# Optimization experiments

Measured on AMD Instinct MI355X. Metric: run time of the kernel, lower is better.

The kernel has to match this reference:

```python
import jax, jax.numpy as jnp
import numpy as np

N = 50000   # total nodes (50 graphs x 1000 nodes)
E = 500000  # total edges (avg degree 10)
G = 50      # number of graphs in the batch
IN = 128    # in_dim
H = 4       # attn_head
HID = [64, 128]  # graph_hiddens
SLOPE = 0.2      # negative_slope


def setup_inputs() -> dict:
    key = jax.random.key(0)
    ks = jax.random.split(key, 12)
    nodes_per_g = N // G
    edges_per_g = E // G
    # edges stay inside their own graph block (batched-graph structure)
    off = (jnp.arange(E) // edges_per_g) * nodes_per_g
    edge_src = (jax.random.randint(ks[0], (E,), 0, nodes_per_g) + off).astype(jnp.int32)
    edge_dst = (jax.random.randint(ks[1], (E,), 0, nodes_per_g) + off).astype(jnp.int32)
    node_graph = (jnp.arange(N) // nodes_per_g).astype(jnp.int32)

    def lin(k, i, o):
        return (jax.random.normal(k, (i, o), jnp.float32) / np.sqrt(i)).astype(jnp.float32)

    return dict(
        x=jax.random.normal(ks[2], (N, IN), jnp.float32),
        edge_src=edge_src, edge_dst=edge_dst, node_graph=node_graph,
        Wl1=lin(ks[3], IN, H * HID[0]), bl1=jnp.zeros((H * HID[0],), jnp.float32),
        Wr1=lin(ks[4], IN, H * HID[0]), br1=jnp.zeros((H * HID[0],), jnp.float32),
        attn1=jax.random.normal(ks[5], (H, HID[0]), jnp.float32) * 0.1,
        Wl2=lin(ks[6], HID[0], H * HID[1]), bl2=jnp.zeros((H * HID[1],), jnp.float32),
        Wr2=lin(ks[7], HID[0], H * HID[1]), br2=jnp.zeros((H * HID[1],), jnp.float32),
        attn2=jax.random.normal(ks[8], (H, HID[1]), jnp.float32) * 0.1,
        gate_w=lin(ks[9], HID[1], 1), gate_b=jnp.zeros((1,), jnp.float32),
    )


def _gat_layer(x, src, dst, Wl, bl, Wr, br, attn, n_heads, d_out):
    """DGL GATv2Conv (share_weights=False, no dropout) + maxpool over heads."""
    n = x.shape[0]
    fs = (x @ Wl + bl).reshape(n, n_heads, d_out)  # fc_src -> [N,H,D]
    fd = (x @ Wr + br).reshape(n, n_heads, d_out)  # fc_dst -> [N,H,D]
    # per-edge GATv2 logits: attn . leaky_relu(fs_u + fd_v)
    e = jax.nn.leaky_relu(fs[src] + fd[dst], SLOPE)      # [E,H,D]
    logits = jnp.einsum('ehd,hd->eh', e, attn)           # [E,H]
    # edge softmax over incoming edges of each destination node
    m = jax.ops.segment_max(logits, dst, num_segments=n)  # [N,H]
    a = jnp.exp(logits - m[dst])
    s = jax.ops.segment_sum(a, dst, num_segments=n)
    alpha = a / s[dst]                                   # [E,H]
    out = jax.ops.segment_sum(alpha[:, :, None] * fs[src], dst, num_segments=n)  # [N,H,D]
    # MaxPool1d(attn_head) over the head dimension -> [N,D]
    return out.max(axis=1)


def reference(x, edge_src, edge_dst, node_graph,
              Wl1, bl1, Wr1, br1, attn1,
              Wl2, bl2, Wr2, br2, attn2,
              gate_w, gate_b):
    h = _gat_layer(x, edge_src, edge_dst, Wl1, bl1, Wr1, br1, attn1, H, HID[0])
    h = _gat_layer(h, edge_src, edge_dst, Wl2, bl2, Wr2, br2, attn2, H, HID[1])
    # GlobalAttentionPooling: softmax(gate_nn(h)) per graph, weighted sum
    gate = (h @ gate_w + gate_b)[:, 0]                      # [N]
    gm = jax.ops.segment_max(gate, node_graph, num_segments=G)
    ga = jnp.exp(gate - gm[node_graph])
    gs = jax.ops.segment_sum(ga, node_graph, num_segments=G)
    alpha = (ga / gs[node_graph])[:, None]                  # [N,1]
    return jax.ops.segment_sum(alpha * h, node_graph, num_segments=G)  # [G, HID[1]]
```

## Files before the change

### kernel.cpp

```cpp
#include <hip/hip_runtime.h>
#include <hip/hip_bf16.h>


#define NN 50000
#define EE 500000
#define GG 50
#define NPG 1000
#define HH 4
#define NB_E ((EE + 255) / 256)
#define NB_W 512

typedef unsigned short ushort_t;
typedef unsigned int uint_t;
typedef __attribute__((ext_vector_type(8))) short bf16x8;
typedef __attribute__((ext_vector_type(4))) float f32x4;
typedef __attribute__((ext_vector_type(2))) float f32x2;

__device__ __forceinline__ ushort_t bf16r(float f) {
  __hip_bfloat16 h = __float2bfloat16(f);
  return *reinterpret_cast<ushort_t*>(&h);
}

__device__ __forceinline__ f32x2 up2v(uint_t u) {
  f32x2 r;
  r.x = __uint_as_float(u << 16);
  r.y = __uint_as_float(u & 0xffff0000u);
  return r;
}


__global__ void prep_count(const int* __restrict__ dst, int* __restrict__ counts,
                           const float* __restrict__ Wl1, const float* __restrict__ Wr1,
                           const float* __restrict__ Wl2, const float* __restrict__ Wr2,
                           ushort_t* __restrict__ BW1, ushort_t* __restrict__ BW2) {
  const int b = blockIdx.x;
  if (b < NB_E) {
    int i = b * 256 + threadIdx.x;
    if (i < EE) atomicAdd(&counts[dst[i]], 1);
  } else {
    int i = (b - NB_E) * 256 + threadIdx.x;
    if (i < 512 * 128) {
      int n = i >> 7, k = i & 127;
      const float* W = (n < 256) ? Wl1 : Wr1;
      BW1[i] = bf16r(W[(size_t)k * 256 + (n & 255)]);
    } else {
      int j = i - 512 * 128;
      int n = j >> 6, k = j & 63;
      const float* W = (n < 512) ? Wl2 : Wr2;
      BW2[j] = bf16r(W[(size_t)k * 512 + (n & 511)]);
    }
  }
}


__global__ void scan_block(const int* __restrict__ in, int* __restrict__ out,
                           int* __restrict__ bsum, int n) {
  __shared__ int tmp[256];
  int t = threadIdx.x;
  int i = blockIdx.x * 256 + t;
  int v = (i < n) ? in[i] : 0;
  tmp[t] = v;
  __syncthreads();
  for (int off = 1; off < 256; off <<= 1) {
    int a = (t >= off) ? tmp[t - off] : 0;
    __syncthreads();
    tmp[t] += a;
    __syncthreads();
  }
  if (i < n) out[i] = tmp[t] - v;
  if (t == 255) bsum[blockIdx.x] = tmp[t];
}

__global__ void scan_bsum(int* __restrict__ bsum, int nb) {
  __shared__ int tmp[256];
  int t = threadIdx.x;
  int v = (t < nb) ? bsum[t] : 0;
  tmp[t] = v;
  __syncthreads();
  for (int off = 1; off < 256; off <<= 1) {
    int a = (t >= off) ? tmp[t - off] : 0;
    __syncthreads();
    tmp[t] += a;
    __syncthreads();
  }
  if (t < nb) bsum[t] = tmp[t] - v;
}

__global__ void scan_add(int* __restrict__ out, const int* __restrict__ bsum,
                         int* __restrict__ cursor, int n) {
  int i = blockIdx.x * 256 + threadIdx.x;
  if (i < n) {
    out[i] += bsum[blockIdx.x];
    cursor[i] = 0;
  }
}

__global__ void scatter_edges(const int* __restrict__ src, const int* __restrict__ dst,
                              const int* __restrict__ rowstart, int* __restrict__ cursor,
                              int* __restrict__ csr_src) {
  int i = blockIdx.x * 256 + threadIdx.x;
  if (i < EE) {
    int d = dst[i];
    int p = atomicAdd(&cursor[d], 1);
    csr_src[rowstart[d] + p] = src[i];
  }
}


template<int KDIM, bool AF32>
__global__ __launch_bounds__(256)
void gemm_mfma(const float* __restrict__ Af, const ushort_t* __restrict__ Ab,
               const ushort_t* __restrict__ BW,
               const float* __restrict__ bl, const float* __restrict__ br, int nhalf,
               ushort_t* __restrict__ C, int nstride) {
  constexpr int RS = 72;
  __shared__ __align__(16) ushort_t As[128 * RS];
  __shared__ __align__(16) ushort_t Bs[128 * RS];
  const int t = threadIdx.x;
  const int m0 = blockIdx.x * 128, n0 = blockIdx.y * 128;
  const int lane = t & 63, wv = t >> 6;
  const int l16 = lane & 15, quad = lane >> 4;

  f32x4 acc[2][8];
#pragma unroll
  for (int b = 0; b < 2; ++b)
#pragma unroll
    for (int n = 0; n < 8; ++n) acc[b][n] = (f32x4){0.f, 0.f, 0.f, 0.f};

  for (int k0 = 0; k0 < KDIM; k0 += 64) {
    __syncthreads();
    if (AF32) {
      const int r = t >> 4, c4 = t & 15;
#pragma unroll
      for (int p = 0; p < 8; ++p) {
        int m = m0 + r + p * 16;
        int ms = (m < NN) ? m : NN - 1;
        float4 v = *(const float4*)(Af + (size_t)ms * KDIM + k0 + c4 * 4);
        uint2 pk;
        pk.x = (uint_t)bf16r(v.x) | ((uint_t)bf16r(v.y) << 16);
        pk.y = (uint_t)bf16r(v.z) | ((uint_t)bf16r(v.w) << 16);
        *(uint2*)(As + (r + p * 16) * RS + c4 * 4) = pk;
      }
    } else {
      const int r = t >> 3, seg = t & 7;
#pragma unroll
      for (int p = 0; p < 4; ++p) {
        int m = m0 + r + p * 32;
        int ms = (m < NN) ? m : NN - 1;
        *(uint4*)(As + (r + p * 32) * RS + seg * 8) =
            *(const uint4*)(Ab + (size_t)ms * KDIM + k0 + seg * 8);
      }
    }
    {
      const int r = t >> 3, seg = t & 7;
#pragma unroll
      for (int p = 0; p < 4; ++p) {
        *(uint4*)(Bs + (r + p * 32) * RS + seg * 8) =
            *(const uint4*)(BW + (size_t)(n0 + r + p * 32) * KDIM + k0 + seg * 8);
      }
    }
    __syncthreads();
#pragma unroll
    for (int kk = 0; kk < 2; ++kk) {
      bf16x8 a[2];
#pragma unroll
      for (int b = 0; b < 2; ++b)
        a[b] = *(const bf16x8*)(As + (wv * 32 + b * 16 + l16) * RS + kk * 32 + quad * 8);
#pragma unroll
      for (int n = 0; n < 8; ++n) {
        bf16x8 bb = *(const bf16x8*)(Bs + (n * 16 + l16) * RS + kk * 32 + quad * 8);
        acc[0][n] = __builtin_amdgcn_mfma_f32_16x16x32_bf16(a[0], bb, acc[0][n], 0, 0, 0);
        acc[1][n] = __builtin_amdgcn_mfma_f32_16x16x32_bf16(a[1], bb, acc[1][n], 0, 0, 0);
      }
    }
  }
  const float* bp = (n0 < nhalf) ? bl : br;
  const int nb = (n0 < nhalf) ? n0 : n0 - nhalf;
#pragma unroll
  for (int n = 0; n < 8; ++n) {
    const int col = n0 + n * 16 + l16;
    const float bv = bp[nb + n * 16 + l16];
#pragma unroll
    for (int b = 0; b < 2; ++b) {
      const int rowb = m0 + wv * 32 + b * 16 + quad * 4;
#pragma unroll
      for (int r = 0; r < 4; ++r) {
        if (rowb + r < NN)
          C[(size_t)(rowb + r) * nstride + col] = bf16r(acc[b][n][r] + bv);
      }
    }
  }
}


template<int N32> struct UV;
template<> struct UV<2> { typedef uint2 T; };
template<> struct UV<4> { typedef uint4 T; };

#define GAT_SLOTS ((NN / 4 + 7) / 8)
#define GAT_GRID  (GAT_SLOTS * 8)

template<int D, int STRIDE, bool OUTBF, bool GATE>
__global__ __launch_bounds__(256)
void gat_layer(const ushort_t* __restrict__ fsb, const ushort_t* __restrict__ fdb,
               const float* __restrict__ attn,
               const int* __restrict__ rowstart, const int* __restrict__ deg,
               const int* __restrict__ csr_src,
               float4* __restrict__ out4, ushort_t* __restrict__ outb,
               const float* __restrict__ gw, float* __restrict__ gate) {
  constexpr int DPL = D / 16;
  constexpr int NU  = DPL / 2;
  constexpr int NV4 = DPL / 4;
  constexpr int D4  = D / 4;
  typedef typename UV<NU>::T LT;

  const int b    = blockIdx.x;
  const int slot = (b & 7) * GAT_SLOTS + (b >> 3);
  if (slot >= NN / 4) return;
  const int lane = threadIdx.x & 63;
  const int wvid = threadIdx.x >> 6;
  const int v    = (slot << 2) + wvid;
  const int h    = lane >> 4;
  const int g16  = lane & 15;
  const int foff = h * D + g16 * DPL;

  f32x2 at2[NU], fd2[NU];
  {
    const float* ap = attn + foff;
#pragma unroll
    for (int j = 0; j < NU; ++j) { at2[j].x = ap[2 * j]; at2[j].y = ap[2 * j + 1]; }
    LT raw = *reinterpret_cast<const LT*>(fdb + (size_t)v * STRIDE + foff);
    const uint_t* rw = reinterpret_cast<const uint_t*>(&raw);
#pragma unroll
    for (int j = 0; j < NU; ++j) fd2[j] = up2v(rw[j]);
  }
  const int start = __builtin_amdgcn_readfirstlane(rowstart[v]);
  const int n     = __builtin_amdgcn_readfirstlane(deg[v]);
  const int* cp   = csr_src + start;

  float s = 0.f;
  f32x2 acc2[NU];
#pragma unroll
  for (int j = 0; j < NU; ++j) acc2[j] = (f32x2){0.f, 0.f};

  if (n > 0) {
    LT raw = *reinterpret_cast<const LT*>(fsb + (size_t)cp[0] * STRIDE + foff);
    for (int e = 1; e <= n; ++e) {
      const LT cur = raw;
      if (e < n)
        raw = *reinterpret_cast<const LT*>(fsb + (size_t)cp[e] * STRIDE + foff);
      const uint_t* rw = reinterpret_cast<const uint_t*>(&cur);
      f32x2 f0[NU];
#pragma unroll
      for (int j = 0; j < NU; ++j) f0[j] = up2v(rw[j]);
      f32x2 p2 = (f32x2){0.f, 0.f};
#pragma unroll
      for (int j = 0; j < NU; ++j) {
        f32x2 t = f0[j] + fd2[j];
        f32x2 l = __builtin_elementwise_max(t, t * 0.2f);
        p2 = __builtin_elementwise_fma(l, at2[j], p2);
      }
      float p = p2.x + p2.y;
      p += __shfl_xor(p, 1);
      p += __shfl_xor(p, 2);
      p += __shfl_xor(p, 4);
      p += __shfl_xor(p, 8);
      const float w = __expf(p);
      s += w;
      const f32x2 wv2 = {w, w};
#pragma unroll
      for (int j = 0; j < NU; ++j)
        acc2[j] = __builtin_elementwise_fma(wv2, f0[j], acc2[j]);
    }
  }

  const float rs = (n > 0) ? (1.0f / s) : 0.f;
  float acc[DPL];
#pragma unroll
  for (int j = 0; j < NU; ++j) {
    acc[2 * j]     = acc2[j].x * rs;
    acc[2 * j + 1] = acc2[j].y * rs;
  }
#pragma unroll
  for (int i = 0; i < DPL; ++i) {
    acc[i] = fmaxf(acc[i], __shfl_xor(acc[i], 16));
    acc[i] = fmaxf(acc[i], __shfl_xor(acc[i], 32));
  }
  if constexpr (GATE) {
    const float* gp = gw + g16 * DPL;
    float g = 0.f;
#pragma unroll
    for (int i = 0; i < DPL; ++i) g = fmaf(acc[i], gp[i], g);
    g += __shfl_xor(g, 1);  g += __shfl_xor(g, 2);  g += __shfl_xor(g, 4);
    g += __shfl_xor(g, 8);  g += __shfl_xor(g, 16); g += __shfl_xor(g, 32);
    if (lane == 0) gate[v] = g * 0.25f;
  }
  if (h == 0) {
    if constexpr (OUTBF) {
      ushort4 o;
      o.x = bf16r(acc[0]); o.y = bf16r(acc[1]); o.z = bf16r(acc[2]); o.w = bf16r(acc[3]);
      *reinterpret_cast<ushort4*>(outb + (size_t)v * D + g16 * 4) = o;
    } else {
#pragma unroll
      for (int i = 0; i < NV4; ++i)
        out4[(size_t)v * D4 + g16 * NV4 + i] =
            make_float4(acc[4 * i], acc[4 * i + 1], acc[4 * i + 2], acc[4 * i + 3]);
    }
  }
}


__global__ __launch_bounds__(1024)
void pool_fused(const float* __restrict__ gate, const float* __restrict__ h2,
                float* __restrict__ out) {
  const int g = blockIdx.x, t = threadIdx.x;
  const int lane = t & 63, w = t >> 6;
  __shared__ float a_s[NPG];
  __shared__ float red[16];
  __shared__ float fin;
  __shared__ float part[8][128];

  float gv = (t < NPG) ? gate[g * NPG + t] : -__builtin_inff();
  float m = gv;
  m = fmaxf(m, __shfl_xor(m, 1));  m = fmaxf(m, __shfl_xor(m, 2));
  m = fmaxf(m, __shfl_xor(m, 4));  m = fmaxf(m, __shfl_xor(m, 8));
  m = fmaxf(m, __shfl_xor(m, 16)); m = fmaxf(m, __shfl_xor(m, 32));
  if (lane == 0) red[w] = m;
  __syncthreads();
  if (t == 0) {
    float r = red[0];
#pragma unroll
    for (int j = 1; j < 16; ++j) r = fmaxf(r, red[j]);
    fin = r;
  }
  __syncthreads();
  const float gm = fin;

  float ex = (t < NPG) ? __expf(gv - gm) : 0.f;
  float s = ex;
  s += __shfl_xor(s, 1);  s += __shfl_xor(s, 2);  s += __shfl_xor(s, 4);
  s += __shfl_xor(s, 8);  s += __shfl_xor(s, 16); s += __shfl_xor(s, 32);
  if (lane == 0) red[w] = s;
  __syncthreads();
  if (t == 0) {
    float r = 0.f;
#pragma unroll
    for (int j = 0; j < 16; ++j) r += red[j];
    fin = 1.0f / r;
  }
  __syncthreads();
  if (t < NPG) a_s[t] = ex * fin;
  __syncthreads();

  const int d = t & 127;
  const int c = t >> 7;
  float acc = 0.f;
  for (int i = c; i < NPG; i += 8)
    acc = fmaf(a_s[i], h2[(size_t)(g * NPG + i) * 128 + d], acc);
  part[c][d] = acc;
  __syncthreads();
  if (c == 0) {
    float r = acc;
#pragma unroll
    for (int j = 1; j < 8; ++j) r += part[j][d];
    out[g * 128 + d] = r;
  }
}


extern "C" void kernel_launch(void* const* d_in, const int* in_sizes, int n_in,
                              void* d_out, int out_size, void* d_ws, size_t ws_size,
                              hipStream_t stream) {
  const float* x        = (const float*)d_in[0];
  const int*   edge_src = (const int*)d_in[1];
  const int*   edge_dst = (const int*)d_in[2];
  const float* Wl1   = (const float*)d_in[4];
  const float* bl1   = (const float*)d_in[5];
  const float* Wr1   = (const float*)d_in[6];
  const float* br1   = (const float*)d_in[7];
  const float* attn1 = (const float*)d_in[8];
  const float* Wl2   = (const float*)d_in[9];
  const float* bl2   = (const float*)d_in[10];
  const float* Wr2   = (const float*)d_in[11];
  const float* br2   = (const float*)d_in[12];
  const float* attn2 = (const float*)d_in[13];
  const float* gate_w = (const float*)d_in[14];
  float* out = (float*)d_out;

  ushort_t* fsd1 = (ushort_t*)d_ws;
  ushort_t* fsd2 = fsd1;
  ushort_t* h1b  = fsd2 + (size_t)NN * 1024;
  float* h2      = (float*)(h1b + (size_t)NN * 64);
  float* gate    = h2 + (size_t)NN * 128;
  ushort_t* BW1  = (ushort_t*)(gate + NN);
  ushort_t* BW2  = BW1 + 512 * 128;
  int* counts   = (int*)(BW2 + 1024 * 64);
  int* rowstart = counts + NN;
  int* cursor   = rowstart + NN;
  int* csr_src  = cursor + NN;
  int* bsum     = csr_src + EE;

  hipMemsetAsync(counts, 0, NN * sizeof(int), stream);

  const int nbN = (NN + 255) / 256;
  const int nbE = NB_E;
  const int MB  = (NN + 127) / 128;

  prep_count<<<NB_E + NB_W, 256, 0, stream>>>(
      edge_dst, counts, Wl1, Wr1, Wl2, Wr2, BW1, BW2);
  scan_block<<<nbN, 256, 0, stream>>>(counts, rowstart, bsum, NN);
  scan_bsum<<<1, 256, 0, stream>>>(bsum, nbN);
  scan_add<<<nbN, 256, 0, stream>>>(rowstart, bsum, cursor, NN);
  scatter_edges<<<nbE, 256, 0, stream>>>(edge_src, edge_dst, rowstart, cursor, csr_src);

  gemm_mfma<128, true><<<dim3(MB, 4), 256, 0, stream>>>(
      x, nullptr, BW1, bl1, br1, 256, fsd1, 512);
  gat_layer<64, 512, true, false><<<GAT_GRID, 256, 0, stream>>>(
      fsd1, fsd1 + 256, attn1, rowstart, counts, csr_src,
      nullptr, h1b, nullptr, nullptr);
  gemm_mfma<64, false><<<dim3(MB, 8), 256, 0, stream>>>(
      nullptr, h1b, BW2, bl2, br2, 512, fsd2, 1024);
  gat_layer<128, 1024, false, true><<<GAT_GRID, 256, 0, stream>>>(
      fsd2, fsd2 + 512, attn2, rowstart, counts, csr_src,
      (float4*)h2, nullptr, gate_w, gate);

  pool_fused<<<GG, 1024, 0, stream>>>(gate, h2, out);
}
```

Before: 377.1 us.

## Split each node's edge list across two wavefronts and combine via LDS

```diff
diff --git a/kernel.cpp b/kernel.cpp
--- a/kernel.cpp
+++ b/kernel.cpp
@@ -197,8 +197,9 @@
 template<> struct UV<2> { typedef uint2 T; };
 template<> struct UV<4> { typedef uint4 T; };
 
-#define GAT_SLOTS ((NN / 4 + 7) / 8)
-#define GAT_GRID  (GAT_SLOTS * 8)
+#define GAT_PAIRS  (NN / 2)
+#define GAT_SLOTSP ((GAT_PAIRS + 7) / 8)
+#define GAT_GRID   (GAT_SLOTSP * 8)
 
 template<int D, int STRIDE, bool OUTBF, bool GATE>
 __global__ __launch_bounds__(256)
@@ -214,12 +215,15 @@
   constexpr int D4  = D / 4;
   typedef typename UV<NU>::T LT;
 
+  __shared__ float part[2][64][DPL + 1];
+
   const int b    = blockIdx.x;
-  const int slot = (b & 7) * GAT_SLOTS + (b >> 3);
-  if (slot >= NN / 4) return;
+  const int pair = (b & 7) * GAT_SLOTSP + (b >> 3);
   const int lane = threadIdx.x & 63;
   const int wvid = threadIdx.x >> 6;
-  const int v    = (slot << 2) + wvid;
+  const int nidx = wvid >> 1;
+  const int half = wvid & 1;
+  const int v    = (pair << 1) + nidx;
   const int h    = lane >> 4;
   const int g16  = lane & 15;
   const int foff = h * D + g16 * DPL;
@@ -234,9 +238,11 @@
 #pragma unroll
     for (int j = 0; j < NU; ++j) fd2[j] = up2v(rw[j]);
   }
-  const int start = __builtin_amdgcn_readfirstlane(rowstart[v]);
-  const int n     = __builtin_amdgcn_readfirstlane(deg[v]);
-  const int* cp   = csr_src + start;
+  const int start_all = __builtin_amdgcn_readfirstlane(rowstart[v]);
+  const int n_all     = __builtin_amdgcn_readfirstlane(deg[v]);
+  const int n0        = (n_all + 1) >> 1;
+  const int n         = half ? (n_all - n0) : n0;
+  const int* cp       = csr_src + start_all + (half ? n0 : 0);
 
   float s = 0.f;
   f32x2 acc2[NU];
@@ -274,7 +280,25 @@
     }
   }
 
-  const float rs = (n > 0) ? (1.0f / s) : 0.f;
+  if (half == 1) {
+#pragma unroll
+    for (int j = 0; j < NU; ++j) {
+      part[nidx][lane][2 * j]     = acc2[j].x;
+      part[nidx][lane][2 * j + 1] = acc2[j].y;
+    }
+    part[nidx][lane][DPL] = s;
+  }
+  __syncthreads();
+  if (half == 1) return;
+
+#pragma unroll
+  for (int j = 0; j < NU; ++j) {
+    acc2[j].x += part[nidx][lane][2 * j];
+    acc2[j].y += part[nidx][lane][2 * j + 1];
+  }
+  s += part[nidx][lane][DPL];
+
+  const float rs = (n_all > 0) ? (1.0f / s) : 0.f;
   float acc[DPL];
 #pragma unroll
   for (int j = 0; j < NU; ++j) {
```

Result: slower. 409.4 us (+8.5%).
